# Kernel optimization log

Measured on AMD Instinct MI355X. Metric: run time of the kernel, lower is better.

The kernel has to match this reference:

```python
import jax, jax.numpy as jnp
import numpy as np

N = 6144       # nodes
E = 12288      # edges (~2N for a sparse simplicial complex)
NF = 32        # node features
EF = 16        # edge features
NH = [32, 32]  # node_hidden
EH = [16, 16]  # edge_hidden
EPS = 1e-5


def setup_inputs() -> dict:
    key = jax.random.key(0)
    ks = jax.random.split(key, 24)
    s = 0.1  # weight init scale
    inp = {}
    inp["X_n"] = jax.random.normal(ks[0], (N, NF), jnp.float32)
    inp["X_e"] = jax.random.normal(ks[1], (E, EF), jnp.float32)
    # normalized adjacency-like operator (non-negative, row mass ~1)
    inp["A_tilde"] = jax.random.uniform(ks[2], (N, N), jnp.float32) * (1.0 / N)
    # normalized Hodge-1 Laplacian-like operator
    inp["L1_tilde"] = jax.random.normal(ks[3], (E, E), jnp.float32) * (1.0 / np.sqrt(E))
    # incidence-like operator
    inp["B1"] = jax.random.normal(ks[4], (N, E), jnp.float32) * (1.0 / np.sqrt(E))
    # GNN linear layers: weight [out, in] (torch convention)
    inp["gnn_W0"] = jax.random.normal(ks[5], (NH[0], NF), jnp.float32) * s
    inp["gnn_b0"] = jnp.zeros((NH[0],), jnp.float32)
    inp["gnn_W1"] = jax.random.normal(ks[6], (NH[1], NH[0]), jnp.float32) * s
    inp["gnn_b1"] = jnp.zeros((NH[1],), jnp.float32)
    # HoSC layer 0: theta in=EF out=EH[0], BN params
    inp["th_W0"] = jax.random.normal(ks[7], (EH[0], EF), jnp.float32) * s
    inp["th_b0"] = jnp.zeros((EH[0],), jnp.float32)
    inp["bn_g0"] = jnp.ones((EH[0],), jnp.float32)
    inp["bn_b0"] = jnp.zeros((EH[0],), jnp.float32)
    # HoSC layer 1: input collapses to 1 channel (max keepdim)
    inp["th_W1"] = jax.random.normal(ks[8], (EH[1], 1), jnp.float32) * s
    inp["th_b1"] = jnp.zeros((EH[1],), jnp.float32)
    inp["bn_g1"] = jnp.ones((EH[1],), jnp.float32)
    inp["bn_b1"] = jnp.zeros((EH[1],), jnp.float32)
    # head: fc1 in = NH[-1] + len(EH) = 34, out = 2N; fc2 out = 1
    inp["fc1_W"] = jax.random.normal(ks[9], (2 * N, NH[-1] + len(EH)), jnp.float32) * s
    inp["fc1_b"] = jnp.zeros((2 * N,), jnp.float32)
    inp["fc2_W"] = jax.random.normal(ks[10], (1, 2 * N), jnp.float32) * s
    inp["fc2_b"] = jnp.zeros((1,), jnp.float32)
    return inp


def _gnn_layer(A, H, W, b):
    # H <- relu((A @ H) @ W^T + b)
    return jax.nn.relu(jnp.matmul(jnp.matmul(A, H), W.T) + b)


def _hosc_layer(Z, L1, W, b, g, beta):
    Zt = jnp.matmul(Z, W.T) + b            # theta
    Zc = jnp.matmul(L1, Zt)                # Laplacian conv
    m = jnp.mean(Zc, axis=0)               # BatchNorm1d (training-mode batch stats)
    v = jnp.var(Zc, axis=0)
    Zp = jax.nn.relu(g * (Zc - m) * jax.lax.rsqrt(v + EPS) + beta)
    return jnp.max(Zp, axis=1, keepdims=True)  # [E, 1]


def reference(X_n, X_e, A_tilde, L1_tilde, B1,
              gnn_W0, gnn_b0, gnn_W1, gnn_b1,
              th_W0, th_b0, bn_g0, bn_b0,
              th_W1, th_b1, bn_g1, bn_b1,
              fc1_W, fc1_b, fc2_W, fc2_b):
    # GNN over nodes
    H = _gnn_layer(A_tilde, X_n, gnn_W0, gnn_b0)
    H_n = _gnn_layer(A_tilde, H, gnn_W1, gnn_b1)      # [N, NH[-1]]
    # HoSC over edges
    Z0 = _hosc_layer(X_e, L1_tilde, th_W0, th_b0, bn_g0, bn_b0)  # [E, 1]
    Z1 = _hosc_layer(Z0, L1_tilde, th_W1, th_b1, bn_g1, bn_b1)   # [E, 1]
    Z_cat = jnp.concatenate([Z0, Z1], axis=1)         # [E, 2]
    H_e = jnp.matmul(B1, Z_cat)                       # [N, 2]
    # head
    Hcat = jnp.concatenate([H_n, H_e], axis=1)        # [N, 34]
    f = jax.nn.relu(jnp.matmul(Hcat, fc1_W.T) + fc1_b)
    f = jnp.matmul(f, fc2_W.T) + fc2_b                # [N, 1]
    return jax.nn.sigmoid(f).squeeze(-1)              # [N]
```

## Files before the change

kernel.cpp:

```cpp
#include <hip/hip_runtime.h>
#include <hip/hip_bf16.h>
#include <math.h>

#define NND 6144
#define NED 12288
static constexpr float EPS_BN = 1e-5f;

#define HN_OFF    0
#define HE_OFF    196608
#define PRE_OFF   208896
#define STATS_OFF 215040
#define Y_OFF     215104
#define T0_OFF    411712
#define T1_OFF    608320
#define Z0_OFF    804928
#define Z1_OFF    817216
#define U_OFF     829504
#define S_OFF     841792

typedef float floatx4 __attribute__((ext_vector_type(4)));

__device__ __forceinline__ float4 ntload4(const float* p) {
  floatx4 v = __builtin_nontemporal_load(reinterpret_cast<const floatx4*>(p));
  return make_float4(v.x, v.y, v.z, v.w);
}
__device__ __forceinline__ float4 ld4(const float* p) {
  return *reinterpret_cast<const float4*>(p);
}

__global__ void init_ws(float* __restrict__ p, int n) {
  int i = blockIdx.x * blockDim.x + threadIdx.x;
  if (i < n) p[i] = 0.f;
}

template<int IC, int OC>
__global__ void small_mm_T(const float* __restrict__ X, const float* __restrict__ W,
                           const float* __restrict__ bias, float* __restrict__ CT, int M) {
  int m = blockIdx.x * blockDim.x + threadIdx.x;
  if (m >= M) return;
  float x[IC];
  #pragma unroll
  for (int k = 0; k < IC; k += 4) {
    float4 v = ld4(X + (size_t)m * IC + k);
    x[k] = v.x; x[k+1] = v.y; x[k+2] = v.z; x[k+3] = v.w;
  }
  #pragma unroll
  for (int oc = 0; oc < OC; ++oc) {
    float s = bias ? bias[oc] : 0.f;
    #pragma unroll
    for (int k = 0; k < IC; ++k) s = fmaf(x[k], W[oc * IC + k], s);
    CT[(size_t)oc * M + m] = s;
  }
}

template<int NC, int CG, bool RELU, bool STATS, bool DBUF>
__global__ __launch_bounds__(256, 3)
void gemm_lds(const float* __restrict__ A, const float* __restrict__ YT,
              const float* __restrict__ bias, float* __restrict__ out,
              float* __restrict__ stats, int K) {
  constexpr int RG = 4 / CG;
  constexpr int ROWS = RG * 4;
  constexpr int SF4 = NC / 4;
  constexpr int NB = DBUF ? 2 : 1;
  __shared__ float Yb[NB][NC][256];
  __shared__ float sst[32];

  const int tid = threadIdx.x;
  const int lane = tid & 63;
  const int w = tid >> 6;
  const int cg = w % CG, rg = w / CG;
  const int r0 = blockIdx.x * ROWS + rg * 4;
  const int c0 = cg * 16;

  const float* ap[4];
  #pragma unroll
  for (int r = 0; r < 4; ++r) ap[r] = A + (size_t)(r0 + r) * K;

  int srow[SF4], scol[SF4];
  #pragma unroll
  for (int i = 0; i < SF4; ++i) {
    int f = tid + 256 * i;
    srow[i] = f >> 6;
    scol[i] = (f & 63) * 4;
  }

  float4 sreg[SF4];
  float acc[4][16];
  #pragma unroll
  for (int r = 0; r < 4; ++r)
    #pragma unroll
    for (int c = 0; c < 16; ++c) acc[r][c] = 0.f;

  auto stage = [&](int kb) {
    #pragma unroll
    for (int i = 0; i < SF4; ++i)
      sreg[i] = ld4(YT + (size_t)srow[i] * K + kb + scol[i]);
  };
  auto dswrite = [&](int b) {
    #pragma unroll
    for (int i = 0; i < SF4; ++i)
      *reinterpret_cast<float4*>(&Yb[b][srow[i]][scol[i]]) = sreg[i];
  };
  auto compute = [&](int b, const float4* av) {
    #pragma unroll
    for (int c = 0; c < 16; ++c) {
      const float4 y = *reinterpret_cast<const float4*>(&Yb[b][c0 + c][lane * 4]);
      #pragma unroll
      for (int r = 0; r < 4; ++r) {
        acc[r][c] = fmaf(av[r].x, y.x, acc[r][c]);
        acc[r][c] = fmaf(av[r].y, y.y, acc[r][c]);
        acc[r][c] = fmaf(av[r].z, y.z, acc[r][c]);
        acc[r][c] = fmaf(av[r].w, y.w, acc[r][c]);
      }
    }
  };

  if (DBUF) {
    stage(0);
    dswrite(0);
    int cur = 0;
    for (int kb = 0; kb < K; kb += 256) {
      const bool more = (kb + 256) < K;
      if (more) stage(kb + 256);
      float4 av[4];
      #pragma unroll
      for (int r = 0; r < 4; ++r) av[r] = ntload4(ap[r] + kb + lane * 4);
      __syncthreads();
      compute(cur, av);
      if (more) dswrite(cur ^ 1);
      cur ^= 1;
    }
  } else {
    for (int kb = 0; kb < K; kb += 256) {
      stage(kb);
      float4 av[4];
      #pragma unroll
      for (int r = 0; r < 4; ++r) av[r] = ntload4(ap[r] + kb + lane * 4);
      __syncthreads();
      dswrite(0);
      __syncthreads();
      compute(0, av);
    }
  }

  float wv[64];
  #pragma unroll
  for (int r = 0; r < 4; ++r)
    #pragma unroll
    for (int c = 0; c < 16; ++c) wv[r * 16 + c] = acc[r][c];
  #pragma unroll
  for (int b = 5; b >= 0; --b) {
    const int m = 1 << b;
    const bool hi = (lane & m) != 0;
    #pragma unroll
    for (int i = 0; i < (1 << b); ++i) {
      float a  = wv[i];
      float bb = wv[i + (1 << b)];
      float send = hi ? a : bb;
      float recv = __shfl_xor(send, m, 64);
      wv[i] = (hi ? bb : a) + recv;
    }
  }

  const int rsel = lane >> 4, csel = lane & 15;
  float v = wv[0] + (bias ? bias[c0 + csel] : 0.f);
  if (RELU) v = fmaxf(v, 0.f);
  out[(size_t)(r0 + rsel) * NC + c0 + csel] = v;

  if (STATS) {
    if (tid < 32) sst[tid] = 0.f;
    __syncthreads();
    float sv = v, qv = v * v;
    sv += __shfl_xor(sv, 16, 64); sv += __shfl_xor(sv, 32, 64);
    qv += __shfl_xor(qv, 16, 64); qv += __shfl_xor(qv, 32, 64);
    if (lane < 16) { atomicAdd(&sst[csel], sv); atomicAdd(&sst[16 + csel], qv); }
    __syncthreads();
    if (tid < 32) atomicAdd(stats + tid, sst[tid]);
  }
}

template<int MODE>
__global__ __launch_bounds__(256)
void rowpass(const float* __restrict__ Mt, const float* __restrict__ za,
             const float* __restrict__ zb, float* __restrict__ o1,
             float* __restrict__ o2, int K) {
  const int lane = threadIdx.x & 63;
  const int row = blockIdx.x * 4 + (threadIdx.x >> 6);
  const float* mp = Mt + (size_t)row * K;
  float accA = 0.f, accB = 0.f;
  for (int kb = 0; kb < K; kb += 512) {
    const int k = kb + lane * 4;
    float4 a0 = ntload4(mp + k);
    float4 a1 = ntload4(mp + k + 256);
    float4 z0 = ld4(za + k);
    float4 z1 = ld4(za + k + 256);
    if (MODE == 0) {
      accA += a0.x*z0.x + a0.y*z0.y + a0.z*z0.z + a0.w*z0.w
            + a1.x*z1.x + a1.y*z1.y + a1.z*z1.z + a1.w*z1.w;
      accB += a0.x + a0.y + a0.z + a0.w + a1.x + a1.y + a1.z + a1.w;
    } else {
      float4 y0 = ld4(zb + k);
      float4 y1 = ld4(zb + k + 256);
      accA += a0.x*z0.x + a0.y*z0.y + a0.z*z0.z + a0.w*z0.w
            + a1.x*z1.x + a1.y*z1.y + a1.z*z1.z + a1.w*z1.w;
      accB += a0.x*y0.x + a0.y*y0.y + a0.z*y0.z + a0.w*y0.w
            + a1.x*y1.x + a1.y*y1.y + a1.z*y1.z + a1.w*y1.w;
    }
  }
  #pragma unroll
  for (int m = 1; m < 64; m <<= 1) {
    accA += __shfl_xor(accA, m, 64);
    accB += __shfl_xor(accB, m, 64);
  }
  if (lane == 0) {
    if (MODE == 0) { o1[row] = accA; o2[row] = accB; }
    else { o1[row * 2] = accA; o1[row * 2 + 1] = accB; }
  }
}

__global__ void bn_max(const float* __restrict__ Zc, const float* __restrict__ stats,
                       const float* __restrict__ g, const float* __restrict__ beta,
                       float* __restrict__ Z, int E) {
  const int e = blockIdx.x * blockDim.x + threadIdx.x;
  if (e >= E) return;
  const float invE = 1.f / (float)E;
  float best = -3.4e38f;
  #pragma unroll
  for (int c = 0; c < 16; ++c) {
    float m = stats[c] * invE;
    float var = stats[16 + c] * invE - m * m;
    float sc = g[c] * rsqrtf(var + EPS_BN);
    float sh = beta[c] - m * sc;
    float x = Zc[(size_t)e * 16 + c];
    best = fmaxf(best, fmaf(x, sc, sh));
  }
  Z[e] = fmaxf(best, 0.f);
}

__global__ void us_stats(const float* __restrict__ u, const float* __restrict__ s,
                         float* __restrict__ st5) {
  const int e = blockIdx.x * 256 + threadIdx.x;
  const int lane = threadIdx.x & 63;
  const int w = threadIdx.x >> 6;
  const float uu = u[e], ss = s[e];
  float v[5] = {uu, ss, uu * uu, ss * ss, uu * ss};
  #pragma unroll
  for (int i = 0; i < 5; ++i)
    #pragma unroll
    for (int m = 1; m < 64; m <<= 1) v[i] += __shfl_xor(v[i], m, 64);
  __shared__ float red[4][5];
  if (lane == 0) {
    #pragma unroll
    for (int i = 0; i < 5; ++i) red[w][i] = v[i];
  }
  __syncthreads();
  if (threadIdx.x < 5) {
    float t = red[0][threadIdx.x] + red[1][threadIdx.x] + red[2][threadIdx.x] + red[3][threadIdx.x];
    atomicAdd(st5 + threadIdx.x, t);
  }
}

__global__ void z1_from_us(const float* __restrict__ u, const float* __restrict__ s,
                           const float* __restrict__ st5,
                           const float* __restrict__ W1, const float* __restrict__ b1,
                           const float* __restrict__ g, const float* __restrict__ beta,
                           float* __restrict__ Z1, int E) {
  const int e = blockIdx.x * blockDim.x + threadIdx.x;
  if (e >= E) return;
  const float invE = 1.f / (float)E;
  const float Su = st5[0], Ss = st5[1], Suu = st5[2], Sss = st5[3], Sus = st5[4];
  const float uu = u[e], ssv = s[e];
  float best = -3.4e38f;
  #pragma unroll
  for (int c = 0; c < 16; ++c) {
    const float wc = W1[c], bc = b1[c];
    const float mean = (wc * Su + bc * Ss) * invE;
    const float ex2 = (wc * wc * Suu + 2.f * wc * bc * Sus + bc * bc * Sss) * invE;
    const float var = ex2 - mean * mean;
    const float sc = g[c] * rsqrtf(var + EPS_BN);
    const float sh = beta[c] - mean * sc;
    best = fmaxf(best, fmaf(wc * uu + bc * ssv, sc, sh));
  }
  Z1[e] = fmaxf(best, 0.f);
}

__global__ __launch_bounds__(256, 2)
void head(const float* __restrict__ Hn, const float* __restrict__ he,
          const float* __restrict__ W1, const float* __restrict__ b1,
          const float* __restrict__ w2, float* __restrict__ pre) {
  const int t = threadIdx.x;
  const int nb = blockIdx.x;
  const int jb = blockIdx.y;
  int n[4];
  float h[4][34];
  float acc[4] = {0.f, 0.f, 0.f, 0.f};
  #pragma unroll
  for (int i = 0; i < 4; ++i) {
    n[i] = nb * 1024 + i * 256 + t;
    #pragma unroll
    for (int k = 0; k < 32; k += 4) {
      float4 v = ld4(Hn + (size_t)n[i] * 32 + k);
      h[i][k] = v.x; h[i][k+1] = v.y; h[i][k+2] = v.z; h[i][k+3] = v.w;
    }
    h[i][32] = he[n[i] * 2];
    h[i][33] = he[n[i] * 2 + 1];
  }
  const int j0 = jb * 192;
  for (int j = j0; j < j0 + 192; ++j) {
    const float* wp = W1 + (size_t)j * 34;
    const float bj = b1[j], vj = w2[j];
    float s0 = bj, s1 = bj, s2 = bj, s3 = bj;
    #pragma unroll
    for (int k = 0; k < 34; ++k) {
      const float wk = wp[k];
      s0 = fmaf(h[0][k], wk, s0); s1 = fmaf(h[1][k], wk, s1);
      s2 = fmaf(h[2][k], wk, s2); s3 = fmaf(h[3][k], wk, s3);
    }
    acc[0] += fmaxf(s0, 0.f) * vj;
    acc[1] += fmaxf(s1, 0.f) * vj;
    acc[2] += fmaxf(s2, 0.f) * vj;
    acc[3] += fmaxf(s3, 0.f) * vj;
  }
  #pragma unroll
  for (int i = 0; i < 4; ++i) atomicAdd(pre + n[i], acc[i]);
}

__global__ void final_k(const float* __restrict__ pre, const float* __restrict__ b2,
                        float* __restrict__ out, int Nn) {
  const int i = blockIdx.x * blockDim.x + threadIdx.x;
  if (i < Nn) out[i] = 1.f / (1.f + expf(-(pre[i] + b2[0])));
}

extern "C" void kernel_launch(void* const* d_in, const int* in_sizes, int n_in,
                              void* d_out, int out_size, void* d_ws, size_t ws_size,
                              hipStream_t stream) {
  const float* X_n   = (const float*)d_in[0];
  const float* X_e   = (const float*)d_in[1];
  const float* A     = (const float*)d_in[2];
  const float* L1    = (const float*)d_in[3];
  const float* B1    = (const float*)d_in[4];
  const float* gW0   = (const float*)d_in[5];
  const float* gb0   = (const float*)d_in[6];
  const float* gW1   = (const float*)d_in[7];
  const float* gb1   = (const float*)d_in[8];
  const float* tW0   = (const float*)d_in[9];
  const float* tb0   = (const float*)d_in[10];
  const float* bng0  = (const float*)d_in[11];
  const float* bnb0  = (const float*)d_in[12];
  const float* tW1   = (const float*)d_in[13];
  const float* tb1   = (const float*)d_in[14];
  const float* bng1  = (const float*)d_in[15];
  const float* bnb1  = (const float*)d_in[16];
  const float* fc1W  = (const float*)d_in[17];
  const float* fc1b  = (const float*)d_in[18];
  const float* fc2W  = (const float*)d_in[19];
  const float* fc2b  = (const float*)d_in[20];

  float* ws   = (float*)d_ws;
  float* Hn   = ws + HN_OFF;
  float* he   = ws + HE_OFF;
  float* pre  = ws + PRE_OFF;
  float* st   = ws + STATS_OFF;
  float* Y    = ws + Y_OFF;
  float* T0   = ws + T0_OFF;
  float* T1   = ws + T1_OFF;
  float* Z0   = ws + Z0_OFF;
  float* Z1   = ws + Z1_OFF;
  float* u    = ws + U_OFF;
  float* s    = ws + S_OFF;
  float* out  = (float*)d_out;

  init_ws<<<25, 256, 0, stream>>>(ws + PRE_OFF, 6208);

  small_mm_T<32, 32><<<24, 256, 0, stream>>>(X_n, gW0, nullptr, Y, NND);
  gemm_lds<32, 2, true, false, false><<<768, 256, 0, stream>>>(A, Y, gb0, T0, nullptr, NND);
  small_mm_T<32, 32><<<24, 256, 0, stream>>>(T0, gW1, nullptr, Y, NND);
  gemm_lds<32, 2, true, false, false><<<768, 256, 0, stream>>>(A, Y, gb1, Hn, nullptr, NND);

  small_mm_T<16, 16><<<48, 256, 0, stream>>>(X_e, tW0, tb0, T1, NED);
  gemm_lds<16, 1, false, true, true><<<768, 256, 0, stream>>>(L1, T1, nullptr, T0, st, NED);
  bn_max<<<48, 256, 0, stream>>>(T0, st, bng0, bnb0, Z0, NED);

  rowpass<0><<<3072, 256, 0, stream>>>(L1, Z0, nullptr, u, s, NED);
  us_stats<<<48, 256, 0, stream>>>(u, s, st + 32);
  z1_from_us<<<48, 256, 0, stream>>>(u, s, st + 32, tW1, tb1, bng1, bnb1, Z1, NED);

  rowpass<1><<<1536, 256, 0, stream>>>(B1, Z0, Z1, he, nullptr, NED);

  head<<<dim3(6, 64), 256, 0, stream>>>(Hn, he, fc1W, fc1b, fc2W, pre);
  final_k<<<24, 256, 0, stream>>>(pre, fc2b, out, NND);
}
```

Before: 631.9 us.

## Prefetch next A tile and Y stage in GEMM, rowpass; replace head atomics with partials

The GEMM kernel drops the separate double-buffered and single-buffer paths. It now uses one LDS buffer and register-prefetches both the next Y stage and the next A rows across the loop, with cached loads for the A=Tilde GEMMs (NT=false). The rowpass kernel register-prefetches the next matrix chunk. The head kernel goes from 4 to 3 nodes per thread with more blocks, and writes per-j-block partial sums instead of atomics, which final_k then reduces. The aim is to hide global-load latency and remove atomic contention, at the cost of extra registers and a 64-way partial-sum buffer.

```diff
diff --git a/kernel.cpp b/kernel.cpp
--- a/kernel.cpp
+++ b/kernel.cpp
@@ -8,15 +8,15 @@
 
 #define HN_OFF    0
 #define HE_OFF    196608
-#define PRE_OFF   208896
-#define STATS_OFF 215040
-#define Y_OFF     215104
-#define T0_OFF    411712
-#define T1_OFF    608320
-#define Z0_OFF    804928
-#define Z1_OFF    817216
-#define U_OFF     829504
-#define S_OFF     841792
+#define ST_OFF    208896
+#define Y_OFF     208960
+#define T0_OFF    405568
+#define T1_OFF    602176
+#define Z0_OFF    798784
+#define Z1_OFF    811072
+#define U_OFF     823360
+#define S_OFF     835648
+#define PP_OFF    847936
 
 typedef float floatx4 __attribute__((ext_vector_type(4)));
 
@@ -53,7 +53,7 @@
   }
 }
 
-template<int NC, int CG, bool RELU, bool STATS, bool DBUF>
+template<int NC, int CG, bool RELU, bool STATS, bool NT>
 __global__ __launch_bounds__(256, 3)
 void gemm_lds(const float* __restrict__ A, const float* __restrict__ YT,
               const float* __restrict__ bias, float* __restrict__ out,
@@ -61,8 +61,7 @@
   constexpr int RG = 4 / CG;
   constexpr int ROWS = RG * 4;
   constexpr int SF4 = NC / 4;
-  constexpr int NB = DBUF ? 2 : 1;
-  __shared__ float Yb[NB][NC][256];
+  __shared__ float Yb[NC][256];
   __shared__ float sst[32];
 
   const int tid = threadIdx.x;
@@ -84,7 +83,7 @@
     scol[i] = (f & 63) * 4;
   }
 
-  float4 sreg[SF4];
+  float4 sreg[SF4], av[4], av2[4];
   float acc[4][16];
   #pragma unroll
   for (int r = 0; r < 4; ++r)
@@ -96,15 +95,30 @@
     for (int i = 0; i < SF4; ++i)
       sreg[i] = ld4(YT + (size_t)srow[i] * K + kb + scol[i]);
   };
-  auto dswrite = [&](int b) {
+  auto loadA = [&](int kb, float4* dst) {
+    #pragma unroll
+    for (int r = 0; r < 4; ++r)
+      dst[r] = NT ? ntload4(ap[r] + kb + lane * 4) : ld4(ap[r] + kb + lane * 4);
+  };
+
+  stage(0);
+  loadA(0, av2);
+
+  for (int kb = 0; kb < K; kb += 256) {
+    __syncthreads();
     #pragma unroll
     for (int i = 0; i < SF4; ++i)
-      *reinterpret_cast<float4*>(&Yb[b][srow[i]][scol[i]]) = sreg[i];
-  };
-  auto compute = [&](int b, const float4* av) {
+      *reinterpret_cast<float4*>(&Yb[srow[i]][scol[i]]) = sreg[i];
+    #pragma unroll
+    for (int r = 0; r < 4; ++r) av[r] = av2[r];
+    if (kb + 256 < K) {
+      stage(kb + 256);
+      loadA(kb + 256, av2);
+    }
+    __syncthreads();
     #pragma unroll
     for (int c = 0; c < 16; ++c) {
-      const float4 y = *reinterpret_cast<const float4*>(&Yb[b][c0 + c][lane * 4]);
+      const float4 y = *reinterpret_cast<const float4*>(&Yb[c0 + c][lane * 4]);
       #pragma unroll
       for (int r = 0; r < 4; ++r) {
         acc[r][c] = fmaf(av[r].x, y.x, acc[r][c]);
@@ -112,34 +126,6 @@
         acc[r][c] = fmaf(av[r].z, y.z, acc[r][c]);
         acc[r][c] = fmaf(av[r].w, y.w, acc[r][c]);
       }
-    }
-  };
-
-  if (DBUF) {
-    stage(0);
-    dswrite(0);
-    int cur = 0;
-    for (int kb = 0; kb < K; kb += 256) {
-      const bool more = (kb + 256) < K;
-      if (more) stage(kb + 256);
-      float4 av[4];
-      #pragma unroll
-      for (int r = 0; r < 4; ++r) av[r] = ntload4(ap[r] + kb + lane * 4);
-      __syncthreads();
-      compute(cur, av);
-      if (more) dswrite(cur ^ 1);
-      cur ^= 1;
-    }
-  } else {
-    for (int kb = 0; kb < K; kb += 256) {
-      stage(kb);
-      float4 av[4];
-      #pragma unroll
-      for (int r = 0; r < 4; ++r) av[r] = ntload4(ap[r] + kb + lane * 4);
-      __syncthreads();
-      dswrite(0);
-      __syncthreads();
-      compute(0, av);
     }
   }
 
@@ -188,10 +174,16 @@
   const int row = blockIdx.x * 4 + (threadIdx.x >> 6);
   const float* mp = Mt + (size_t)row * K;
   float accA = 0.f, accB = 0.f;
+  float4 a0 = ntload4(mp + lane * 4);
+  float4 a1 = ntload4(mp + 256 + lane * 4);
   for (int kb = 0; kb < K; kb += 512) {
     const int k = kb + lane * 4;
-    float4 a0 = ntload4(mp + k);
-    float4 a1 = ntload4(mp + k + 256);
+    float4 n0, n1;
+    const bool more = (kb + 512) < K;
+    if (more) {
+      n0 = ntload4(mp + k + 512);
+      n1 = ntload4(mp + k + 768);
+    }
     float4 z0 = ld4(za + k);
     float4 z1 = ld4(za + k + 256);
     if (MODE == 0) {
@@ -206,6 +198,7 @@
       accB += a0.x*y0.x + a0.y*y0.y + a0.z*y0.z + a0.w*y0.w
             + a1.x*y1.x + a1.y*y1.y + a1.z*y1.z + a1.w*y1.w;
     }
+    if (more) { a0 = n0; a1 = n1; }
   }
   #pragma unroll
   for (int m = 1; m < 64; m <<= 1) {
@@ -287,48 +280,53 @@
 __global__ __launch_bounds__(256, 2)
 void head(const float* __restrict__ Hn, const float* __restrict__ he,
           const float* __restrict__ W1, const float* __restrict__ b1,
-          const float* __restrict__ w2, float* __restrict__ pre) {
+          const float* __restrict__ w2, float* __restrict__ prepart) {
   const int t = threadIdx.x;
   const int nb = blockIdx.x;
   const int jb = blockIdx.y;
-  int n[4];
-  float h[4][34];
-  float acc[4] = {0.f, 0.f, 0.f, 0.f};
-  #pragma unroll
-  for (int i = 0; i < 4; ++i) {
-    n[i] = nb * 1024 + i * 256 + t;
+  int n[3];
+  float h[3][34];
+  float acc[3] = {0.f, 0.f, 0.f};
+  #pragma unroll
+  for (int i = 0; i < 3; ++i) {
+    n[i] = nb * 768 + i * 256 + t;
     #pragma unroll
     for (int k = 0; k < 32; k += 4) {
       float4 v = ld4(Hn + (size_t)n[i] * 32 + k);
       h[i][k] = v.x; h[i][k+1] = v.y; h[i][k+2] = v.z; h[i][k+3] = v.w;
     }
-    h[i][32] = he[n[i] * 2];
-    h[i][33] = he[n[i] * 2 + 1];
+    float2 e2 = *reinterpret_cast<const float2*>(he + n[i] * 2);
+    h[i][32] = e2.x;
+    h[i][33] = e2.y;
   }
   const int j0 = jb * 192;
   for (int j = j0; j < j0 + 192; ++j) {
     const float* wp = W1 + (size_t)j * 34;
     const float bj = b1[j], vj = w2[j];
-    float s0 = bj, s1 = bj, s2 = bj, s3 = bj;
+    float s0 = bj, s1 = bj, s2 = bj;
     #pragma unroll
     for (int k = 0; k < 34; ++k) {
       const float wk = wp[k];
-      s0 = fmaf(h[0][k], wk, s0); s1 = fmaf(h[1][k], wk, s1);
-      s2 = fmaf(h[2][k], wk, s2); s3 = fmaf(h[3][k], wk, s3);
+      s0 = fmaf(h[0][k], wk, s0);
+      s1 = fmaf(h[1][k], wk, s1);
+      s2 = fmaf(h[2][k], wk, s2);
     }
     acc[0] += fmaxf(s0, 0.f) * vj;
     acc[1] += fmaxf(s1, 0.f) * vj;
     acc[2] += fmaxf(s2, 0.f) * vj;
-    acc[3] += fmaxf(s3, 0.f) * vj;
-  }
-  #pragma unroll
-  for (int i = 0; i < 4; ++i) atomicAdd(pre + n[i], acc[i]);
-}
-
-__global__ void final_k(const float* __restrict__ pre, const float* __restrict__ b2,
+  }
+  #pragma unroll
+  for (int i = 0; i < 3; ++i) prepart[(size_t)jb * NND + n[i]] = acc[i];
+}
+
+__global__ void final_k(const float* __restrict__ pp, const float* __restrict__ b2,
                         float* __restrict__ out, int Nn) {
   const int i = blockIdx.x * blockDim.x + threadIdx.x;
-  if (i < Nn) out[i] = 1.f / (1.f + expf(-(pre[i] + b2[0])));
+  if (i >= Nn) return;
+  float s = 0.f;
+  #pragma unroll
+  for (int j = 0; j < 64; ++j) s += pp[(size_t)j * NND + i];
+  out[i] = 1.f / (1.f + expf(-(s + b2[0])));
 }
 
 extern "C" void kernel_launch(void* const* d_in, const int* in_sizes, int n_in,
@@ -359,8 +357,7 @@
   float* ws   = (float*)d_ws;
   float* Hn   = ws + HN_OFF;
   float* he   = ws + HE_OFF;
-  float* pre  = ws + PRE_OFF;
-  float* st   = ws + STATS_OFF;
+  float* st   = ws + ST_OFF;
   float* Y    = ws + Y_OFF;
   float* T0   = ws + T0_OFF;
   float* T1   = ws + T1_OFF;
@@ -368,9 +365,10 @@
   float* Z1   = ws + Z1_OFF;
   float* u    = ws + U_OFF;
   float* s    = ws + S_OFF;
+  float* pp   = ws + PP_OFF;
   float* out  = (float*)d_out;
 
-  init_ws<<<25, 256, 0, stream>>>(ws + PRE_OFF, 6208);
+  init_ws<<<1, 64, 0, stream>>>(st, 64);
 
   small_mm_T<32, 32><<<24, 256, 0, stream>>>(X_n, gW0, nullptr, Y, NND);
   gemm_lds<32, 2, true, false, false><<<768, 256, 0, stream>>>(A, Y, gb0, T0, nullptr, NND);
@@ -387,6 +385,6 @@
 
   rowpass<1><<<1536, 256, 0, stream>>>(B1, Z0, Z1, he, nullptr, NED);
 
-  head<<<dim3(6, 64), 256, 0, stream>>>(Hn, he, fc1W, fc1b, fc2W, pre);
-  final_k<<<24, 256, 0, stream>>>(pre, fc2b, out, NND);
-}
+  head<<<dim3(8, 64), 256, 0, stream>>>(Hn, he, fc1W, fc1b, fc2W, pp);
+  final_k<<<24, 256, 0, stream>>>(pp, fc2b, out, NND);
+}
```

Measured after the change: 610.5 us. 1.03x faster.
